# Optimization experiments

Hardware: AMD Instinct MI355X
Metric: run time of the kernel (lower is better)

Reference implementation:

```python
import jax, jax.numpy as jnp
import numpy as np

HID, H, P, N, G, K = 2688, 64, 64, 128, 8, 4
I = H * P            # intermediate_size = 4096
GN = G * N           # groups_ssm_state_size = 1024
CONV_DIM = I + 2 * GN  # 6144
TOTAL = 2 * I + 2 * GN + H  # 10304
EPS = 1e-5


def setup_inputs() -> dict:
    key = jax.random.key(0)
    ks = jax.random.split(key, 8)
    B, T = 2, 2048
    hidden_states = jax.random.normal(ks[0], (B, T, HID), dtype=jnp.float32)
    in_proj_w = jax.random.normal(ks[1], (TOTAL, HID), dtype=jnp.float32) * 0.02
    conv_w = jax.random.normal(ks[2], (CONV_DIM, K), dtype=jnp.float32) * 0.1  # depthwise kernel
    conv_b = jnp.zeros((CONV_DIM,), dtype=jnp.float32)
    A = -jnp.exp(jax.random.normal(ks[3], (H,), dtype=jnp.float32))
    D = jnp.ones((H,), dtype=jnp.float32)
    dt_bias = jnp.ones((H,), dtype=jnp.float32)
    norm_weight = jnp.ones((I,), dtype=jnp.float32)
    out_proj_w = jax.random.normal(ks[4], (HID, I), dtype=jnp.float32) * 0.02
    return {"hidden_states": hidden_states, "in_proj_w": in_proj_w, "conv_w": conv_w,
            "conv_b": conv_b, "A": A, "D": D, "dt_bias": dt_bias,
            "norm_weight": norm_weight, "out_proj_w": out_proj_w}


def reference(hidden_states, in_proj_w, conv_w, conv_b, A, D, dt_bias, norm_weight, out_proj_w):
    B, T, _ = hidden_states.shape
    hpg = H // G  # heads per group

    # 1-2. in_proj and split
    proj = jnp.einsum('bth,oh->bto', hidden_states, in_proj_w)  # (B,T,TOTAL)
    gate = proj[..., :I]
    xBC = proj[..., I:I + CONV_DIM]
    dt = proj[..., I + CONV_DIM:]  # (B,T,H)

    # 3. causal depthwise conv1d (left-pad K-1, slice to T) + silu
    xp = jnp.pad(xBC, ((0, 0), (K - 1, 0), (0, 0)))
    conv = conv_b
    for i in range(K):  # tiny fixed kernel loop
        conv = conv + xp[:, i:i + T, :] * conv_w[:, i]
    conv = jax.nn.silu(conv)

    # 4-5. split and reshape
    x = conv[..., :I].reshape(B, T, H, P)
    Bm = conv[..., I:I + GN].reshape(B, T, G, N)
    Cm = conv[..., I + GN:].reshape(B, T, G, N)

    # 6. selective scan (precompute dt / A_bar outside the scan)
    dt_sp = jax.nn.softplus(dt + dt_bias)          # (B,T,H)
    A_bar = jnp.exp(A * dt_sp)                     # (B,T,H)
    xg = x.reshape(B, T, G, hpg, P)
    Ab = A_bar.reshape(B, T, G, hpg)
    dts = dt_sp.reshape(B, T, G, hpg)

    def step(h, inp):
        x_t, B_t, C_t, Ab_t, dt_t = inp  # (B,G,hpg,P),(B,G,N),(B,G,N),(B,G,hpg),(B,G,hpg)
        outer = dt_t[..., None, None] * x_t[..., None] * B_t[:, :, None, None, :]
        h = Ab_t[..., None, None] * h + outer      # (B,G,hpg,P,N)
        y_t = jnp.einsum('bghpn,bgn->bghp', h, C_t)
        return h, y_t

    inputs = (jnp.moveaxis(xg, 1, 0), jnp.moveaxis(Bm, 1, 0), jnp.moveaxis(Cm, 1, 0),
              jnp.moveaxis(Ab, 1, 0), jnp.moveaxis(dts, 1, 0))
    h0 = jnp.zeros((B, G, hpg, P, N), dtype=hidden_states.dtype)
    _, ys = jax.lax.scan(step, h0, inputs)         # (T,B,G,hpg,P)
    y = jnp.moveaxis(ys, 0, 1).reshape(B, T, H, P) + D[None, None, :, None] * x
    y = y.reshape(B, T, I)

    # 7. gated RMSNorm
    y = y * jax.nn.silu(gate)
    var = jnp.mean(y * y, axis=-1, keepdims=True)
    y = y * jax.lax.rsqrt(var + EPS) * norm_weight

    # 8. out_proj
    return jnp.einsum('bti,oi->bto', y, out_proj_w)
```

## Files before the change

### kernel.cpp

```cpp
#include <hip/hip_runtime.h>
#include <stdint.h>

typedef unsigned short ushort_t;
typedef __attribute__((ext_vector_type(4))) float f32x4;
typedef __attribute__((ext_vector_type(2))) float f32x2;
typedef __attribute__((ext_vector_type(8))) __bf16 bf16x8;
typedef __attribute__((ext_vector_type(4))) unsigned short u16x4;
typedef __attribute__((ext_vector_type(8))) unsigned short u16x8;

#define DEV __device__ __forceinline__

DEV void gload_lds16(const void* g, void* l) {
  __builtin_amdgcn_global_load_lds(
      (const __attribute__((address_space(1))) uint32_t*)(uintptr_t)(g),
      (__attribute__((address_space(3))) uint32_t*)(uintptr_t)(l), 16, 0, 0);
}

DEV ushort_t f2bf(float f) {
  union { float f; uint32_t u; } x; x.f = f;
  x.u += 0x7fffu + ((x.u >> 16) & 1u);
  return (ushort_t)(x.u >> 16);
}

DEV float bf2f(ushort_t u) {
  union { uint32_t u; float f; } x; x.u = (uint32_t)u << 16; return x.f;
}

DEV float siluf(float x) { return x / (1.f + expf(-x)); }

DEV float fexp2(float x) {
#if __has_builtin(__builtin_amdgcn_exp2f)
  return __builtin_amdgcn_exp2f(x);
#else
  return exp2f(x);
#endif
}

#define BAR asm volatile("s_barrier" ::: "memory")
#define LGKM0 do { asm volatile("s_waitcnt lgkmcnt(0)" ::: "memory"); \
                   __builtin_amdgcn_sched_barrier(0); } while (0)
#define VMCNT(n) asm volatile("s_waitcnt vmcnt(" #n ")" ::: "memory")

__global__ __launch_bounds__(256) void fill_kernel(float* p, float v, int n) {
  int i = blockIdx.x * 256 + threadIdx.x;
  if (i < n) p[i] = v;
}

__global__ __launch_bounds__(256) void cvt_bf16_kernel(const float* __restrict__ src,
                                                       ushort_t* __restrict__ dst,
                                                       int n_src4, int n_dst4) {
  int i = blockIdx.x * 256 + threadIdx.x;
  if (i >= n_dst4) return;
  f32x4 v;
  if (i < n_src4) v = *(const f32x4*)(src + (size_t)i * 4);
  else { v.x = 0.f; v.y = 0.f; v.z = 0.f; v.w = 0.f; }
  u16x4 o;
  o.x = f2bf(v.x); o.y = f2bf(v.y); o.z = f2bf(v.z); o.w = f2bf(v.w);
  *(u16x4*)(dst + (size_t)i * 4) = o;
}

DEV void ld_a4(const unsigned char* ab2, int mgofs, int ck0, int ck1, bf16x8 (&af)[4][2]) {
#pragma unroll
  for (int mi = 0; mi < 4; ++mi) {
    const unsigned char* p = ab2 + (mgofs + mi * 16) * 128;
    af[mi][0] = *(const bf16x8*)(p + ck0);
    af[mi][1] = *(const bf16x8*)(p + ck1);
  }
}

DEV void ld_b2(const unsigned char* bb2, int npofs, int ck0, int ck1, bf16x8 (&bf)[2][2]) {
#pragma unroll
  for (int ni = 0; ni < 2; ++ni) {
    const unsigned char* p = bb2 + (npofs + ni * 16) * 128;
    bf[ni][0] = *(const bf16x8*)(p + ck0);
    bf[ni][1] = *(const bf16x8*)(p + ck1);
  }
}

DEV void mm16(f32x4 (&acc)[8][4], const bf16x8 (&af)[4][2], const bf16x8 (&bf)[2][2],
              int mb, int nb) {
  __builtin_amdgcn_s_setprio(1);
#pragma unroll
  for (int mi = 0; mi < 4; ++mi)
#pragma unroll
    for (int ni = 0; ni < 2; ++ni)
#pragma unroll
      for (int kk = 0; kk < 2; ++kk)
        acc[mb + mi][nb + ni] = __builtin_amdgcn_mfma_f32_16x16x32_bf16(
            af[mi][kk], bf[ni][kk], acc[mb + mi][nb + ni], 0, 0, 0);
  __builtin_amdgcn_s_setprio(0);
}

DEV void stage2(const ushort_t* s0, const ushort_t* s1, unsigned char* d) {
  gload_lds16(s0, d);
  gload_lds16(s1, d + 8192);
}

template <int MODE>
__global__ __launch_bounds__(512, 1) void gemm8_kernel(const ushort_t* __restrict__ A,
                                                       const ushort_t* __restrict__ B,
                                                       void* __restrict__ C0,
                                                       void* __restrict__ C1,
                                                       int K, int NB, int NC, int niter) {
  __shared__ __align__(16) unsigned char lds[131072];
  const int tid = threadIdx.x;
  const int l = tid & 63, w = tid >> 6;
  const int wr = w >> 2, wc = w & 3;
  const int lr = l & 15, lk = l >> 4;
  const int xm = (lr & 7) << 4;
  const int ck0 = (lk * 16) ^ xm;
  const int ck1 = (64 + lk * 16) ^ xm;
  const int bm = blockIdx.x, bn = blockIdx.y;

  const int rr = (w << 3) + (l >> 3);
  const int cE = ((l & 7) ^ (l >> 3)) << 3;
  const int dstoff = w * 1024 + l * 16;

  const ushort_t* sA00 = A + (size_t)(bm * 256 +       rr) * K + cE;
  const ushort_t* sA01 = A + (size_t)(bm * 256 +  64 + rr) * K + cE;
  const ushort_t* sA10 = A + (size_t)(bm * 256 + 128 + rr) * K + cE;
  const ushort_t* sA11 = A + (size_t)(bm * 256 + 192 + rr) * K + cE;
  int rb0 = bn * 256 +       rr; if (rb0 > NB - 1) rb0 = NB - 1;
  int rb1 = bn * 256 +  64 + rr; if (rb1 > NB - 1) rb1 = NB - 1;
  int rb2 = bn * 256 + 128 + rr; if (rb2 > NB - 1) rb2 = NB - 1;
  int rb3 = bn * 256 + 192 + rr; if (rb3 > NB - 1) rb3 = NB - 1;
  const ushort_t* sB00 = B + (size_t)rb0 * K + cE;
  const ushort_t* sB01 = B + (size_t)rb1 * K + cE;
  const ushort_t* sB10 = B + (size_t)rb2 * K + cE;
  const ushort_t* sB11 = B + (size_t)rb3 * K + cE;

  const int aoff = wr * 16384 + lr * 128;
  const int boff = 32768 + (wc >> 1) * 16384 + ((wc & 1) * 64 + lr) * 128;

  f32x4 acc[8][4] = {};
  bf16x8 af[4][2], bf[2][2], bg[2][2];

  stage2(sA00, sA01, lds + dstoff);
  stage2(sA10, sA11, lds + 16384 + dstoff);
  stage2(sB00, sB01, lds + 32768 + dstoff);
  stage2(sB10, sB11, lds + 49152 + dstoff);
  stage2(sA00 + 64, sA01 + 64, lds + 65536 + dstoff);
  VMCNT(2);
  BAR;

  auto kpair = [&](int kt0, bool last) {
    const unsigned char* a0 = lds + aoff;
    const unsigned char* b0 = lds + boff;
    const unsigned char* a1 = lds + 65536 + aoff;
    const unsigned char* b1 = lds + 65536 + boff;
    const size_t c1 = (size_t)(kt0 + 1) * 64;
    const size_t c2 = (size_t)(kt0 + 2) * 64;
    const size_t c3 = (size_t)(kt0 + 3) * 64;
    ld_a4(a0, 0, ck0, ck1, af);
    ld_b2(b0, 0, ck0, ck1, bf);
    stage2(sA10 + c1, sA11 + c1, lds + 65536 + 16384 + dstoff);
    BAR; LGKM0; mm16(acc, af, bf, 0, 0); BAR;
    ld_b2(b0, 32, ck0, ck1, bg);
    stage2(sB00 + c1, sB01 + c1, lds + 65536 + 32768 + dstoff);
    BAR; LGKM0; mm16(acc, af, bg, 0, 2); BAR;
    ld_a4(a0, 64, ck0, ck1, af);
    stage2(sB10 + c1, sB11 + c1, lds + 65536 + 49152 + dstoff);
    BAR; LGKM0; mm16(acc, af, bg, 4, 2); BAR;
    if (!last) { stage2(sA00 + c2, sA01 + c2, lds + dstoff); VMCNT(2); }
    else       { VMCNT(0); }
    BAR; LGKM0; mm16(acc, af, bf, 4, 0); BAR;
    ld_a4(a1, 0, ck0, ck1, af);
    ld_b2(b1, 0, ck0, ck1, bf);
    if (!last) stage2(sA10 + c2, sA11 + c2, lds + 16384 + dstoff);
    BAR; LGKM0; mm16(acc, af, bf, 0, 0); BAR;
    ld_b2(b1, 32, ck0, ck1, bg);
    if (!last) stage2(sB00 + c2, sB01 + c2, lds + 32768 + dstoff);
    BAR; LGKM0; mm16(acc, af, bg, 0, 2); BAR;
    ld_a4(a1, 64, ck0, ck1, af);
    if (!last) stage2(sB10 + c2, sB11 + c2, lds + 49152 + dstoff);
    BAR; LGKM0; mm16(acc, af, bg, 4, 2); BAR;
    if (!last) { stage2(sA00 + c3, sA01 + c3, lds + 65536 + dstoff); VMCNT(2); }
    BAR; LGKM0; mm16(acc, af, bf, 4, 0); BAR;
  };

  for (int it = 0; it < niter - 1; ++it) kpair(2 * it, false);
  kpair(2 * (niter - 1), true);

  if (MODE == 0) {
#pragma unroll
    for (int mi = 0; mi < 8; ++mi)
#pragma unroll
      for (int ni = 0; ni < 4; ++ni)
#pragma unroll
        for (int r = 0; r < 4; ++r) {
          const int row = wr * 128 + mi * 16 + (lk << 2) + r;
          const int cb = (wc * 64 + ni * 16 + lr) * 2;
          *(ushort_t*)(lds + row * 512 + (cb ^ ((row & 7) << 4))) =
              f2bf(acc[mi][ni][r]);
        }
    LGKM0; BAR;
    ushort_t* dstb; size_t stride; int cbase;
    if (bn < 16) { dstb = (ushort_t*)C0; stride = 4096; cbase = bn * 256; }
    else         { dstb = (ushort_t*)C1; stride = 6272; cbase = bn * 256 - 4096; }
    const int lc = l & 31;
    const bool okc = (bn * 256 + lc * 8) < NC;
#pragma unroll
    for (int it = 0; it < 16; ++it) {
      const int row = w * 32 + it * 2 + (l >> 5);
      u16x8 v = *(const u16x8*)(lds + row * 512 + ((lc * 16) ^ ((row & 7) << 4)));
      if (okc)
        *(u16x8*)(dstb + (size_t)(bm * 256 + row) * stride + cbase + lc * 8) = v;
    }
  } else {
    float* o = (float*)C0;
    const bool okc = (bn * 256 + l * 4) < NC;
#pragma unroll
    for (int h2 = 0; h2 < 2; ++h2) {
      if (h2) { LGKM0; BAR; }
      if (wr == h2) {
#pragma unroll
        for (int mi = 0; mi < 8; ++mi)
#pragma unroll
          for (int ni = 0; ni < 4; ++ni)
#pragma unroll
            for (int r = 0; r < 4; ++r) {
              const int rl = mi * 16 + (lk << 2) + r;
              const int cb = (wc * 64 + ni * 16 + lr) * 4;
              *(float*)(lds + rl * 1024 + (cb ^ ((rl & 7) << 4))) = acc[mi][ni][r];
            }
      }
      LGKM0; BAR;
#pragma unroll
      for (int it = 0; it < 16; ++it) {
        const int rl = w * 16 + it;
        f32x4 v = *(const f32x4*)(lds + rl * 1024 + ((l * 16) ^ ((rl & 7) << 4)));
        if (okc)
          *(f32x4*)(o + (size_t)(bm * 256 + h2 * 128 + rl) * NC + bn * 256 + l * 4) = v;
      }
    }
  }
}

__global__ __launch_bounds__(256) void conv_silu_kernel(const ushort_t* __restrict__ xbc,
                                                        const float* __restrict__ cw,
                                                        const float* __restrict__ cb,
                                                        ushort_t* __restrict__ out) {
  int idx = blockIdx.x * 256 + threadIdx.x;
  int c4 = (idx % 1536) << 2;
  int bt = idx / 1536;
  int t = bt & 2047;
  const ushort_t* base = xbc + (size_t)bt * 6272 + c4;
  f32x4 w0 = *(const f32x4*)&cw[(c4 + 0) * 4];
  f32x4 w1 = *(const f32x4*)&cw[(c4 + 1) * 4];
  f32x4 w2 = *(const f32x4*)&cw[(c4 + 2) * 4];
  f32x4 w3 = *(const f32x4*)&cw[(c4 + 3) * 4];
  f32x4 acc = *(const f32x4*)&cb[c4];
#pragma unroll
  for (int i = 0; i < 4; ++i) {
    int dt_ = i - 3;
    if (t + dt_ >= 0) {
      u16x4 xv = *(const u16x4*)(base + (ptrdiff_t)dt_ * 6272);
      acc.x += bf2f(xv.x) * w0[i];
      acc.y += bf2f(xv.y) * w1[i];
      acc.z += bf2f(xv.z) * w2[i];
      acc.w += bf2f(xv.w) * w3[i];
    }
  }
  u16x4 o;
  o.x = f2bf(siluf(acc.x)); o.y = f2bf(siluf(acc.y));
  o.z = f2bf(siluf(acc.z)); o.w = f2bf(siluf(acc.w));
  *(u16x4*)(out + (size_t)bt * 6144 + c4) = o;
}

__global__ __launch_bounds__(256) void dt_kernel(const ushort_t* __restrict__ xbc,
                                                 const float* __restrict__ dt_bias,
                                                 const float* __restrict__ Avec,
                                                 float* __restrict__ dtA) {
  int idx = blockIdx.x * 256 + threadIdx.x;
  int h = idx >> 12, bt = idx & 4095;
  float v = bf2f(xbc[(size_t)bt * 6272 + 6144 + h]) + dt_bias[h];
  float sp = fmaxf(v, 0.f) + log1pf(expf(-fabsf(v)));
  float ab = expf(Avec[h] * sp);
  dtA[(h << 13) + bt] = sp;
  dtA[(h << 13) + 4096 + bt] = ab;
}

__global__ __launch_bounds__(256) void ssd_kernel(const ushort_t* __restrict__ conv,
                                                  const float* __restrict__ dtA,
                                                  const float* __restrict__ Dvec,
                                                  const float* __restrict__ Avec,
                                                  ushort_t* __restrict__ yssm,
                                                  ushort_t* __restrict__ hst,
                                                  float* __restrict__ abprod) {
  const int bid = blockIdx.x;
  const int ck = bid & 7;
  const int h = (bid >> 3) & 63;
  const int b = bid >> 9;
  const int g = h >> 3;
  const int tid = threadIdx.x;
  const int lane = tid & 63;
  const int wv = tid >> 6;
  const int lr = lane & 15, lk = lane >> 4;
  const int btb = (b << 11) + (ck << 8);

  __shared__ __align__(16) unsigned char ldsb[69648];
  float* csL = (float*)(ldsb + 65536);
  float* dtL = (float*)(ldsb + 66560);
  float* wL  = (float*)(ldsb + 67584);
  float* l2L = (float*)(ldsb + 68608);
  float* wsum = (float*)(ldsb + 69632);

  const float Ah = Avec[h];
  const float Dh = Dvec[h];
  const float AhL2 = Ah * 1.44269504f;

  float dv = dtA[(h << 13) + btb + tid];
  float s = dv;
#pragma unroll
  for (int off = 1; off < 64; off <<= 1) {
    float t = __shfl_up(s, off, 64);
    if (lane >= off) s += t;
  }
  if (lane == 63) wsum[wv] = s;
  __syncthreads();
  float basev = 0.f;
  for (int i = 0; i < wv; ++i) basev += wsum[i];
  const float csv = basev + s;
  csL[tid] = csv;
  dtL[tid] = dv;
  l2L[tid] = AhL2 * csv;
  __syncthreads();
  const float cstot = csL[255];
  wL[tid] = dv * fexp2(AhL2 * (cstot - csv));
  if (tid == 0) abprod[((b << 6) + h) * 8 + ck] = expf(Ah * cstot);

  const ushort_t* Xg = conv + (size_t)btb * 6144 + (h << 6);
  {
    const int p = lane;
#pragma unroll
    for (int rep = 0; rep < 8; ++rep) {
      const int t0 = (rep * 4 + wv) << 3;
      u16x8 v;
#pragma unroll
      for (int k = 0; k < 8; ++k) v[k] = Xg[(size_t)(t0 + k) * 6144 + p];
      *(u16x8*)(ldsb + p * 512 + ((t0 * 2) ^ ((p & 15) << 4))) = v;
    }
  }
  __syncthreads();

  const ushort_t* Bg = conv + (size_t)btb * 6144 + 4096 + (g << 7);
  f32x4 hacc[4][2] = {};
  for (int th = 0; th < 2; ++th) {
#pragma unroll
    for (int rep = 0; rep < 8; ++rep) {
      const int n = ((rep & 1) << 6) | lane;
      const int tl0 = ((rep >> 1) * 4 + wv) << 3;
      const int t0 = th * 128 + tl0;
      u16x8 v;
#pragma unroll
      for (int k = 0; k < 8; ++k)
        v[k] = f2bf(bf2f(Bg[(size_t)(t0 + k) * 6144 + n]) * wL[t0 + k]);
      *(u16x8*)(ldsb + 32768 + n * 256 + ((tl0 * 2) ^ ((n & 15) << 4))) = v;
    }
    __syncthreads();
#pragma unroll
    for (int tc = 0; tc < 4; ++tc) {
      bf16x8 a4[4], b2[2];
#pragma unroll
      for (int pf = 0; pf < 4; ++pf) {
        const int p = pf * 16 + lr;
        a4[pf] = *(const bf16x8*)(ldsb + p * 512 +
                                  (((th * 128 + tc * 32 + lk * 8) * 2) ^ ((p & 15) << 4)));
      }
#pragma unroll
      for (int nf = 0; nf < 2; ++nf) {
        const int n = wv * 32 + nf * 16 + lr;
        b2[nf] = *(const bf16x8*)(ldsb + 32768 + n * 256 +
                                  (((tc * 32 + lk * 8) * 2) ^ ((n & 15) << 4)));
      }
#pragma unroll
      for (int pf = 0; pf < 4; ++pf)
#pragma unroll
        for (int nf = 0; nf < 2; ++nf)
          hacc[pf][nf] = __builtin_amdgcn_mfma_f32_16x16x32_bf16(a4[pf], b2[nf],
                                                                 hacc[pf][nf], 0, 0, 0);
    }
    __syncthreads();
  }
#pragma unroll
  for (int pf = 0; pf < 4; ++pf)
#pragma unroll
    for (int nf = 0; nf < 2; ++nf)
#pragma unroll
      for (int r = 0; r < 4; ++r) {
        int p = pf * 16 + (lk << 2) + r;
        int n = wv * 32 + nf * 16 + lr;
        hst[((size_t)((b << 10) | (h << 4) | ((p >> 5) << 3) | ck)) * 4096 +
            (size_t)(p & 31) * 128 + n] = f2bf(hacc[pf][nf][r]);
      }

  const ushort_t* Cg = conv + (size_t)btb * 6144 + 5120 + (g << 7);
  for (int rb = 0; rb < 4; ++rb) {
    const int i0 = rb << 6;
    f32x4 sacc[4][4] = {};
#pragma unroll
    for (int kk = 0; kk < 4; ++kk) {
      bf16x8 ca[4], bb[4];
#pragma unroll
      for (int ifr = 0; ifr < 4; ++ifr)
        ca[ifr] = *(const bf16x8*)(Cg + (size_t)(i0 + ifr * 16 + lr) * 6144 + kk * 32 + lk * 8);
#pragma unroll
      for (int jf = 0; jf < 4; ++jf)
        bb[jf] = *(const bf16x8*)(Bg + (size_t)(wv * 64 + jf * 16 + lr) * 6144 + kk * 32 + lk * 8);
#pragma unroll
      for (int ifr = 0; ifr < 4; ++ifr)
#pragma unroll
        for (int jf = 0; jf < 4; ++jf)
          sacc[ifr][jf] = __builtin_amdgcn_mfma_f32_16x16x32_bf16(ca[ifr], bb[jf],
                                                                  sacc[ifr][jf], 0, 0, 0);
    }
#pragma unroll
    for (int ifr = 0; ifr < 4; ++ifr) {
      const int ibmax = i0 + ifr * 16 + 15;
#pragma unroll
      for (int jf = 0; jf < 4; ++jf) {
        const int jbmin = wv * 64 + jf * 16;
        const int j = jbmin + lr;
        if (jbmin > ibmax) {
#pragma unroll
          for (int r = 0; r < 4; ++r) {
            int il = ifr * 16 + (lk << 2) + r;
            *(ushort_t*)(ldsb + 32768 + il * 512 + ((j * 2) ^ ((il & 15) << 4))) = 0;
          }
        } else {
          const float dtj = dtL[j];
          const float l2j = l2L[j];
#pragma unroll
          for (int r = 0; r < 4; ++r) {
            int il = ifr * 16 + (lk << 2) + r;
            int ig = i0 + il;
            float val = 0.f;
            if (j <= ig) val = sacc[ifr][jf][r] * dtj * fexp2(l2L[ig] - l2j);
            *(ushort_t*)(ldsb + 32768 + il * 512 + ((j * 2) ^ ((il & 15) << 4))) = f2bf(val);
          }
        }
      }
    }
    __syncthreads();
    f32x4 yacc[4] = {};
    const int ilB = wv * 16 + lr;
#pragma unroll
    for (int ks = 0; ks < 8; ++ks) {
      bf16x8 pb = *(const bf16x8*)(ldsb + 32768 + ilB * 512 +
                                   (((ks * 32 + lk * 8) * 2) ^ ((ilB & 15) << 4)));
#pragma unroll
      for (int pf = 0; pf < 4; ++pf) {
        const int p = pf * 16 + lr;
        bf16x8 pa = *(const bf16x8*)(ldsb + p * 512 +
                                     (((ks * 32 + lk * 8) * 2) ^ ((p & 15) << 4)));
        yacc[pf] = __builtin_amdgcn_mfma_f32_16x16x32_bf16(pa, pb, yacc[pf], 0, 0, 0);
      }
    }
    const int irow = i0 + wv * 16 + lr;
    const size_t ybase = (size_t)(btb + irow) * 4096 + (h << 6);
#pragma unroll
    for (int pf = 0; pf < 4; ++pf) {
      u16x4 o;
#pragma unroll
      for (int r = 0; r < 4; ++r) {
        int p = pf * 16 + (lk << 2) + r;
        float xv = bf2f(*(const ushort_t*)(ldsb + p * 512 +
                                           ((irow * 2) ^ ((p & 15) << 4))));
        o[r] = f2bf(yacc[pf][r] + Dh * xv);
      }
      *(u16x4*)(yssm + ybase + pf * 16 + (lk << 2)) = o;
    }
    __syncthreads();
  }
}

__global__ __launch_bounds__(256) void combine_kernel(ushort_t* __restrict__ hst,
                                                      const float* __restrict__ abprod) {
  const int bid = blockIdx.x;
  const int bh = bid >> 1;
  const int tid = threadIdx.x;
  const size_t base = (size_t)bid * 8 * 4096 + tid * 16;
  float hrun[16];
#pragma unroll
  for (int e = 0; e < 16; ++e) hrun[e] = 0.f;
  for (int c = 0; c < 8; ++c) {
    const size_t p = base + (size_t)c * 4096;
    u16x8 v0 = *(const u16x8*)&hst[p];
    u16x8 v1 = *(const u16x8*)&hst[p + 8];
    float ab = abprod[bh * 8 + c];
    u16x8 w0, w1;
#pragma unroll
    for (int e = 0; e < 8; ++e) { w0[e] = f2bf(hrun[e]); w1[e] = f2bf(hrun[8 + e]); }
    *(u16x8*)&hst[p] = w0;
    *(u16x8*)&hst[p + 8] = w1;
#pragma unroll
    for (int e = 0; e < 8; ++e) {
      hrun[e] = ab * hrun[e] + bf2f(v0[e]);
      hrun[8 + e] = ab * hrun[8 + e] + bf2f(v1[e]);
    }
  }
}

__global__ __launch_bounds__(256) void correct_kernel(const ushort_t* __restrict__ conv,
                                                      const float* __restrict__ dtA,
                                                      const float* __restrict__ Avec,
                                                      const ushort_t* __restrict__ hst,
                                                      ushort_t* __restrict__ yssm) {
  const int bid = blockIdx.x;
  const int ck = bid & 7;
  const int h = (bid >> 3) & 63;
  const int b = bid >> 9;
  const int g = h >> 3;
  const int tid = threadIdx.x;
  const int lane = tid & 63;
  const int w = tid >> 6;
  const int lr = lane & 15, lk = lane >> 4;
  const int btb = (b << 11) + (ck << 8);

  __shared__ float pdl[256];
  __shared__ float wsum[4];
  float s = dtA[(h << 13) + btb + tid];
#pragma unroll
  for (int off = 1; off < 64; off <<= 1) {
    float t = __shfl_up(s, off, 64);
    if (lane >= off) s += t;
  }
  if (lane == 63) wsum[w] = s;
  __syncthreads();
  float basev = 0.f;
  for (int i = 0; i < w; ++i) basev += wsum[i];
  pdl[tid] = expf(Avec[h] * (basev + s));
  __syncthreads();

  const ushort_t* Cc = conv + (size_t)btb * 6144 + 5120 + (g << 7);
  const size_t hb0 = ((size_t)((b << 10) | (h << 4) | (0 << 3) | ck)) * 4096;
  const size_t hb1 = ((size_t)((b << 10) | (h << 4) | (1 << 3) | ck)) * 4096;

  f32x4 acc[4][4] = {};
#pragma unroll
  for (int kk = 0; kk < 4; ++kk) {
    const int k0 = kk * 32 + lk * 8;
    bf16x8 afr[4], bfr[4];
#pragma unroll
    for (int mf = 0; mf < 4; ++mf) {
      const int t = w * 64 + mf * 16 + lr;
      afr[mf] = *(const bf16x8*)(Cc + (size_t)t * 6144 + k0);
    }
#pragma unroll
    for (int nf = 0; nf < 4; ++nf) {
      const int p = nf * 16 + lr;
      const size_t hb = (p < 32) ? hb0 : hb1;
      bfr[nf] = *(const bf16x8*)(hst + hb + (size_t)(p & 31) * 128 + k0);
    }
#pragma unroll
    for (int mf = 0; mf < 4; ++mf)
#pragma unroll
      for (int nf = 0; nf < 4; ++nf)
        acc[mf][nf] = __builtin_amdgcn_mfma_f32_16x16x32_bf16(afr[mf], bfr[nf],
                                                              acc[mf][nf], 0, 0, 0);
  }

#pragma unroll
  for (int mf = 0; mf < 4; ++mf) {
#pragma unroll
    for (int r = 0; r < 4; ++r) {
      const int row = w * 64 + mf * 16 + (lk << 2) + r;
      const float pd = pdl[row];
      const size_t yrow = (size_t)(btb + row) * 4096 + (h << 6);
#pragma unroll
      for (int nf = 0; nf < 4; ++nf) {
        const int p = nf * 16 + lr;
        const size_t idx = yrow + p;
        yssm[idx] = f2bf(bf2f(yssm[idx]) + pd * acc[mf][nf][r]);
      }
    }
  }
}

__global__ __launch_bounds__(256) void norm_kernel(const ushort_t* __restrict__ yssm,
                                                   const ushort_t* __restrict__ gate,
                                                   const float* __restrict__ nw,
                                                   ushort_t* __restrict__ out) {
  const int bt = blockIdx.x;
  const int tid = threadIdx.x;
  const ushort_t* y = yssm + (size_t)bt * 4096;
  const ushort_t* gt = gate + (size_t)bt * 4096;
  float vals[16];
  float ss = 0.f;
#pragma unroll
  for (int j = 0; j < 4; ++j) {
    int o = (tid + j * 256) << 2;
    u16x4 yv = *(const u16x4*)(y + o);
    u16x4 gv = *(const u16x4*)(gt + o);
#pragma unroll
    for (int e = 0; e < 4; ++e) {
      float v = bf2f(yv[e]) * siluf(bf2f(gv[e]));
      vals[j * 4 + e] = v;
      ss += v * v;
    }
  }
#pragma unroll
  for (int m = 1; m <= 32; m <<= 1) ss += __shfl_xor(ss, m, 64);
  __shared__ float red[4];
  if ((tid & 63) == 0) red[tid >> 6] = ss;
  __syncthreads();
  ss = red[0] + red[1] + red[2] + red[3];
  const float sc = rsqrtf(ss * (1.f / 4096.f) + 1e-5f);
#pragma unroll
  for (int j = 0; j < 4; ++j) {
    int o = (tid + j * 256) << 2;
    f32x4 wv = *(const f32x4*)(nw + o);
    u16x4 ov;
    ov.x = f2bf(vals[j * 4 + 0] * sc * wv.x);
    ov.y = f2bf(vals[j * 4 + 1] * sc * wv.y);
    ov.z = f2bf(vals[j * 4 + 2] * sc * wv.z);
    ov.w = f2bf(vals[j * 4 + 3] * sc * wv.w);
    *(u16x4*)(out + (size_t)bt * 4096 + o) = ov;
  }
}

extern "C" void kernel_launch(void* const* d_in, const int* in_sizes, int n_in,
                              void* d_out, int out_size, void* d_ws, size_t ws_size,
                              hipStream_t stream) {
  const float* hidden  = (const float*)d_in[0];
  const float* w_in    = (const float*)d_in[1];
  const float* conv_w  = (const float*)d_in[2];
  const float* conv_b  = (const float*)d_in[3];
  const float* Avec    = (const float*)d_in[4];
  const float* Dvec    = (const float*)d_in[5];
  const float* dt_bias = (const float*)d_in[6];
  const float* nw      = (const float*)d_in[7];
  const float* w_out   = (const float*)d_in[8];
  float* out = (float*)d_out;

  char* ws = (char*)d_ws;
  ushort_t* Xbf   = (ushort_t*)(ws);
  ushort_t* W1bf  = (ushort_t*)(ws + 22020096);
  ushort_t* gate  = (ushort_t*)(ws + 77758464);
  ushort_t* xbc   = (ushort_t*)(ws + 111312896);
  ushort_t* W2bf  = Xbf;
  ushort_t* convb = W1bf;
  float*    dtA   = (float*)(ws + 22020096 + 50331648);
  float*    abprod= (float*)(ws + 22020096 + 52428800);
  ushort_t* yssm  = xbc;
  ushort_t* hst   = (ushort_t*)(ws + 111312896 + 33554432);
  ushort_t* ynorm = convb;
  const size_t NEED = 162693120;
  if (NEED > ws_size) {
    fill_kernel<<<4, 256, 0, stream>>>(out, 12345.0f, 1024);
    return;
  }

  cvt_bf16_kernel<<<10752, 256, 0, stream>>>(hidden, Xbf, 2752512, 2752512);
  cvt_bf16_kernel<<<27216, 256, 0, stream>>>(w_in, W1bf, 6924288, 6967296);
  gemm8_kernel<0><<<dim3(16, 41), 512, 0, stream>>>(Xbf, W1bf, gate, xbc,
                                                    2688, 10368, 10304, 21);
  cvt_bf16_kernel<<<10752, 256, 0, stream>>>(w_out, W2bf, 2752512, 2752512);
  conv_silu_kernel<<<24576, 256, 0, stream>>>(xbc, conv_w, conv_b, convb);
  dt_kernel<<<1024, 256, 0, stream>>>(xbc, dt_bias, Avec, dtA);
  ssd_kernel<<<1024, 256, 0, stream>>>(convb, dtA, Dvec, Avec, yssm, hst, abprod);
  combine_kernel<<<256, 256, 0, stream>>>(hst, abprod);
  correct_kernel<<<1024, 256, 0, stream>>>(convb, dtA, Avec, hst, yssm);
  norm_kernel<<<4096, 256, 0, stream>>>(yssm, gate, nw, ynorm);
  gemm8_kernel<1><<<dim3(16, 11), 512, 0, stream>>>(ynorm, W2bf, out, nullptr,
                                                    4096, 2688, 2688, 32);
}
```

Before: 658.2 us.

## Restructure GEMM k-loop into four 32-MFMA phases with reordered prefetch

Replaces the eight 16-MFMA phases per k-pair with four 32-MFMA phases. Both B fragment halves are held in registers at once, so each A fragment load covers the full N slice. Global-to-LDS prefetches are regrouped so B tiles are staged ahead of A tiles with matching vmcnt waits. The goal is to halve barrier and LDS-wait overhead per k step, at the cost of more live registers and a changed load/compute overlap pattern.

```diff
diff --git a/kernel.cpp b/kernel.cpp
--- a/kernel.cpp
+++ b/kernel.cpp
@@ -77,17 +77,22 @@
   }
 }
 
-DEV void mm16(f32x4 (&acc)[8][4], const bf16x8 (&af)[4][2], const bf16x8 (&bf)[2][2],
-              int mb, int nb) {
+DEV void mm32(f32x4 (&acc)[8][4], const bf16x8 (&af)[4][2], const bf16x8 (&bl)[2][2],
+              const bf16x8 (&bh)[2][2], int mb) {
   __builtin_amdgcn_s_setprio(1);
 #pragma unroll
   for (int mi = 0; mi < 4; ++mi)
 #pragma unroll
-    for (int ni = 0; ni < 2; ++ni)
-#pragma unroll
-      for (int kk = 0; kk < 2; ++kk)
-        acc[mb + mi][nb + ni] = __builtin_amdgcn_mfma_f32_16x16x32_bf16(
-            af[mi][kk], bf[ni][kk], acc[mb + mi][nb + ni], 0, 0, 0);
+    for (int kk = 0; kk < 2; ++kk) {
+#pragma unroll
+      for (int ni = 0; ni < 2; ++ni)
+        acc[mb + mi][ni] = __builtin_amdgcn_mfma_f32_16x16x32_bf16(
+            af[mi][kk], bl[ni][kk], acc[mb + mi][ni], 0, 0, 0);
+#pragma unroll
+      for (int ni = 0; ni < 2; ++ni)
+        acc[mb + mi][2 + ni] = __builtin_amdgcn_mfma_f32_16x16x32_bf16(
+            af[mi][kk], bh[ni][kk], acc[mb + mi][2 + ni], 0, 0, 0);
+    }
   __builtin_amdgcn_s_setprio(0);
 }
 
@@ -133,14 +138,15 @@
   const int boff = 32768 + (wc >> 1) * 16384 + ((wc & 1) * 64 + lr) * 128;
 
   f32x4 acc[8][4] = {};
-  bf16x8 af[4][2], bf[2][2], bg[2][2];
+  bf16x8 af[4][2], bfl[2][2], bfh[2][2];
 
   stage2(sA00, sA01, lds + dstoff);
   stage2(sA10, sA11, lds + 16384 + dstoff);
   stage2(sB00, sB01, lds + 32768 + dstoff);
   stage2(sB10, sB11, lds + 49152 + dstoff);
-  stage2(sA00 + 64, sA01 + 64, lds + 65536 + dstoff);
-  VMCNT(2);
+  stage2(sB00 + 64, sB01 + 64, lds + 65536 + 32768 + dstoff);
+  stage2(sB10 + 64, sB11 + 64, lds + 65536 + 49152 + dstoff);
+  VMCNT(4);
   BAR;
 
   auto kpair = [&](int kt0, bool last) {
@@ -152,30 +158,35 @@
     const size_t c2 = (size_t)(kt0 + 2) * 64;
     const size_t c3 = (size_t)(kt0 + 3) * 64;
     ld_a4(a0, 0, ck0, ck1, af);
-    ld_b2(b0, 0, ck0, ck1, bf);
+    ld_b2(b0, 0, ck0, ck1, bfl);
+    ld_b2(b0, 32, ck0, ck1, bfh);
+    stage2(sA00 + c1, sA01 + c1, lds + 65536 + dstoff);
     stage2(sA10 + c1, sA11 + c1, lds + 65536 + 16384 + dstoff);
-    BAR; LGKM0; mm16(acc, af, bf, 0, 0); BAR;
-    ld_b2(b0, 32, ck0, ck1, bg);
-    stage2(sB00 + c1, sB01 + c1, lds + 65536 + 32768 + dstoff);
-    BAR; LGKM0; mm16(acc, af, bg, 0, 2); BAR;
+    BAR; LGKM0; mm32(acc, af, bfl, bfh, 0); BAR;
     ld_a4(a0, 64, ck0, ck1, af);
-    stage2(sB10 + c1, sB11 + c1, lds + 65536 + 49152 + dstoff);
-    BAR; LGKM0; mm16(acc, af, bg, 4, 2); BAR;
-    if (!last) { stage2(sA00 + c2, sA01 + c2, lds + dstoff); VMCNT(2); }
-    else       { VMCNT(0); }
-    BAR; LGKM0; mm16(acc, af, bf, 4, 0); BAR;
+    if (!last) {
+      stage2(sB00 + c2, sB01 + c2, lds + 32768 + dstoff);
+      stage2(sB10 + c2, sB11 + c2, lds + 49152 + dstoff);
+      VMCNT(4);
+    } else {
+      VMCNT(0);
+    }
+    BAR; LGKM0; mm32(acc, af, bfl, bfh, 4); BAR;
     ld_a4(a1, 0, ck0, ck1, af);
-    ld_b2(b1, 0, ck0, ck1, bf);
-    if (!last) stage2(sA10 + c2, sA11 + c2, lds + 16384 + dstoff);
-    BAR; LGKM0; mm16(acc, af, bf, 0, 0); BAR;
-    ld_b2(b1, 32, ck0, ck1, bg);
-    if (!last) stage2(sB00 + c2, sB01 + c2, lds + 32768 + dstoff);
-    BAR; LGKM0; mm16(acc, af, bg, 0, 2); BAR;
+    ld_b2(b1, 0, ck0, ck1, bfl);
+    ld_b2(b1, 32, ck0, ck1, bfh);
+    if (!last) {
+      stage2(sA00 + c2, sA01 + c2, lds + dstoff);
+      stage2(sA10 + c2, sA11 + c2, lds + 16384 + dstoff);
+    }
+    BAR; LGKM0; mm32(acc, af, bfl, bfh, 0); BAR;
     ld_a4(a1, 64, ck0, ck1, af);
-    if (!last) stage2(sB10 + c2, sB11 + c2, lds + 49152 + dstoff);
-    BAR; LGKM0; mm16(acc, af, bg, 4, 2); BAR;
-    if (!last) { stage2(sA00 + c3, sA01 + c3, lds + 65536 + dstoff); VMCNT(2); }
-    BAR; LGKM0; mm16(acc, af, bf, 4, 0); BAR;
+    if (!last) {
+      stage2(sB00 + c3, sB01 + c3, lds + 65536 + 32768 + dstoff);
+      stage2(sB10 + c3, sB11 + c3, lds + 65536 + 49152 + dstoff);
+      VMCNT(4);
+    }
+    BAR; LGKM0; mm32(acc, af, bfl, bfh, 4); BAR;
   };
 
   for (int it = 0; it < niter - 1; ++it) kpair(2 * it, false);
```

New measurement: 657.5 us. Within noise of the previous version (-0.1%).
